# Optimization experiments

Hardware: AMD Instinct MI355X
Metric: run time of the kernel (lower is better)

## Reference

```python
import jax, jax.numpy as jnp
import numpy as np

N, F_IN, H, C = 100000, 256, 128, 64
E, EP = 1600000, 500000


def setup_inputs() -> dict:
    key = jax.random.key(0)
    ks = jax.random.split(key, 8)
    x = jax.random.normal(ks[0], (N, F_IN), jnp.float32)
    masked_nodes = jax.random.randint(ks[1], (1000,), 0, N)
    pos_edge_index = jax.random.randint(ks[2], (2, EP), 0, N)
    neg_edge_index = jax.random.randint(ks[3], (2, EP), 0, N)
    edge_index = jax.random.randint(ks[4], (2, E), 0, N)
    W1 = jax.random.normal(ks[5], (F_IN, H), jnp.float32) / np.sqrt(F_IN).astype(np.float32)
    b1 = jnp.zeros((H,), jnp.float32)
    W2 = jax.random.normal(ks[6], (H, C), jnp.float32) / np.sqrt(H).astype(np.float32)
    b2 = jnp.zeros((C,), jnp.float32)
    return dict(x=x, masked_nodes=masked_nodes, pos_edge_index=pos_edge_index,
                neg_edge_index=neg_edge_index, edge_index=edge_index,
                W1=W1, b1=b1, W2=W2, b2=b2)


def gcn_conv(x, W, b, src, dst, n):
    # PyG GCNConv: h = x @ W; symmetric norm with self-loops; aggregate; + bias
    h = x @ W  # [N, out]
    deg = jax.ops.segment_sum(jnp.ones(src.shape[0], h.dtype), dst, num_segments=n) + 1.0
    dis = jax.lax.rsqrt(deg)  # D^{-1/2} including self-loop
    msg = h[src] * (dis[src] * dis[dst])[:, None]           # gather + edge-norm
    agg = jax.ops.segment_sum(msg, dst, num_segments=n)      # scatter-add
    agg = agg + h * (dis * dis)[:, None]                      # self-loop term
    return agg + b


def reference(x, masked_nodes, pos_edge_index, neg_edge_index, edge_index, W1, b1, W2, b2):
    n = x.shape[0]
    src, dst = edge_index[0], edge_index[1]
    h = jax.nn.relu(gcn_conv(x, W1, b1, src, dst, n))
    h = gcn_conv(h, W2, b2, src, dst, n)  # [N, C]
    tei = jnp.concatenate([pos_edge_index, neg_edge_index], axis=-1)  # [2, 2*EP]
    x_j = h[tei[0]]  # [2EP, C]
    x_i = h[tei[1]]
    scores = jnp.einsum('ef,ef->e', x_i, x_j)
    return scores, jnp.zeros(tei.shape, jnp.float32)
```

## Files before the change

kernel.cpp:

```cpp
#include <hip/hip_runtime.h>

#define N_NODES 100000
#define F_IN    256
#define H_DIM   128
#define C_DIM   64
#define E_EDGES 1600000
#define EP_EDGES 500000

#define NBUK 391
#define EPB  4096

typedef unsigned short bf16_t;
typedef short  short8  __attribute__((ext_vector_type(8)));
typedef float  float4v __attribute__((ext_vector_type(4)));

__device__ inline bf16_t f2bf(float f) {
    unsigned u = __float_as_uint(f);
    u += 0x7fff + ((u >> 16) & 1);
    return (bf16_t)(u >> 16);
}
__device__ inline float bf2f(bf16_t h) {
    return __uint_as_float(((unsigned)h) << 16);
}
__device__ inline void split8(const float* vv, short* h, short* l) {
#pragma unroll
    for (int j = 0; j < 8; ++j) {
        bf16_t hb = f2bf(vv[j]);
        h[j] = (short)hb;
        l[j] = (short)f2bf(vv[j] - bf2f(hb));
    }
}
__device__ inline float4v mfma16(short8 a, short8 b, float4v c) {
    return __builtin_amdgcn_mfma_f32_16x16x32_bf16(a, b, c, 0, 0, 0);
}

__global__ __launch_bounds__(256) void hist_kernel(const int* __restrict__ dst,
                                                   int* __restrict__ counts) {
    int e = blockIdx.x * 256 + threadIdx.x;
    if (e < E_EDGES) atomicAdd(&counts[dst[e]], 1);
}

__global__ __launch_bounds__(256) void dis_kernel(const int* __restrict__ counts,
                                                  float* __restrict__ dis) {
    int i = blockIdx.x * 256 + threadIdx.x;
    if (i < N_NODES) dis[i] = rsqrtf((float)counts[i] + 1.0f);
}

__global__ __launch_bounds__(256) void scan1_kernel(const int* __restrict__ counts,
                                                    int* __restrict__ row_ptr,
                                                    int* __restrict__ blocksum) {
    __shared__ int sh[256];
    int t = threadIdx.x;
    int i = blockIdx.x * 256 + t;
    int v = (i < N_NODES) ? counts[i] : 0;
    sh[t] = v;
    __syncthreads();
#pragma unroll
    for (int off = 1; off < 256; off <<= 1) {
        int u = (t >= off) ? sh[t - off] : 0;
        __syncthreads();
        sh[t] += u;
        __syncthreads();
    }
    if (i < N_NODES) row_ptr[i + 1] = sh[t];
    if (t == 255) blocksum[blockIdx.x] = sh[255];
}

__global__ __launch_bounds__(512) void scan2_kernel(int* __restrict__ blocksum, int nb) {
    __shared__ int sh[512];
    int t = threadIdx.x;
    sh[t] = (t < nb) ? blocksum[t] : 0;
    __syncthreads();
#pragma unroll
    for (int off = 1; off < 512; off <<= 1) {
        int u = (t >= off) ? sh[t - off] : 0;
        __syncthreads();
        sh[t] += u;
        __syncthreads();
    }
    if (t < nb) blocksum[t] = (t == 0) ? 0 : sh[t - 1];
}

__global__ __launch_bounds__(256) void scan3_kernel(int* __restrict__ row_ptr,
                                                    const int* __restrict__ blocksum) {
    int i = blockIdx.x * 256 + threadIdx.x;
    if (i >= N_NODES) return;
    row_ptr[i + 1] += blocksum[blockIdx.x];
    if (i == 0) row_ptr[0] = 0;
}

__global__ __launch_bounds__(512) void binit_kernel(const int* __restrict__ row_ptr,
                                                    int* __restrict__ bcursor) {
    int b = threadIdx.x;
    if (b < NBUK) bcursor[b] = row_ptr[b << 8];
}

__global__ __launch_bounds__(256) void bucket_scatter_kernel(const int* __restrict__ src,
                                                             const int* __restrict__ dst,
                                                             int* __restrict__ bcursor,
                                                             int2* __restrict__ pairs) {
    __shared__ int hist[NBUK];
    __shared__ int base[NBUK];
    const int t = threadIdx.x;
    for (int b = t; b < NBUK; b += 256) hist[b] = 0;
    __syncthreads();

    const int e0 = blockIdx.x * EPB;
    int s[16], d[16];
#pragma unroll
    for (int i = 0; i < 16; ++i) {
        int e = e0 + i * 256 + t;
        if (e < E_EDGES) {
            s[i] = src[e];
            d[i] = dst[e];
            atomicAdd(&hist[d[i] >> 8], 1);
        } else {
            d[i] = -1;
        }
    }
    __syncthreads();
    for (int b = t; b < NBUK; b += 256) {
        int c = hist[b];
        base[b] = c ? atomicAdd(&bcursor[b], c) : 0;
        hist[b] = 0;
    }
    __syncthreads();
#pragma unroll
    for (int i = 0; i < 16; ++i) {
        if (d[i] >= 0) {
            int b = d[i] >> 8;
            int r = atomicAdd(&hist[b], 1);
            pairs[base[b] + r] = make_int2(s[i], d[i]);
        }
    }
}

__global__ __launch_bounds__(256) void bucket_sort_kernel(const int2* __restrict__ pairs,
                                                          const int* __restrict__ row_ptr,
                                                          int* __restrict__ csr_src) {
    __shared__ int cursor[256];
    const int b = blockIdx.x;
    const int node0 = b << 8;
    const int t = threadIdx.x;
    const int nn = min(256, N_NODES - node0);
    if (t < nn) cursor[t] = row_ptr[node0 + t];
    __syncthreads();
    const int beg = row_ptr[node0];
    const int end = row_ptr[node0 + nn];
    for (int e = beg + t; e < end; e += 256) {
        int2 p = pairs[e];
        int j = atomicAdd(&cursor[p.y - node0], 1);
        csr_src[j] = p.x;
    }
}

__global__ __launch_bounds__(256) void wprep_kernel(const float* __restrict__ W1,
                                                    const float* __restrict__ W2,
                                                    short* __restrict__ w1h,
                                                    short* __restrict__ w1l,
                                                    short* __restrict__ w2h,
                                                    short* __restrict__ w2l) {
    int idx = blockIdx.x * 256 + threadIdx.x;
    if (idx < H_DIM * F_IN) {
        int n = idx >> 8, k = idx & 255;
        float w = W1[k * H_DIM + n];
        bf16_t h = f2bf(w);
        w1h[idx] = (short)h;
        w1l[idx] = (short)f2bf(w - bf2f(h));
    }
    int i2 = idx - H_DIM * F_IN;
    if (i2 >= 0 && i2 < C_DIM * H_DIM) {
        int n = i2 >> 7, k = i2 & 127;
        float w = W2[k * C_DIM + n];
        bf16_t h = f2bf(w);
        w2h[i2] = (short)h;
        w2l[i2] = (short)f2bf(w - bf2f(h));
    }
}

__global__ __launch_bounds__(256) void gemm1_mfma(const float* __restrict__ X,
                                                  const short* __restrict__ Wth,
                                                  const short* __restrict__ Wtl,
                                                  bf16_t* __restrict__ T,
                                                  int nrows) {
    __shared__ short Ah[128 * 48], Al[128 * 48];
    __shared__ short Bh[128 * 48], Bl[128 * 48];
    const int t = threadIdx.x;
    const int row0 = blockIdx.x * 128;
    const int w = t >> 6;
    const int lane = t & 63;
    const int m = lane & 15;
    const int q = lane >> 4;
    const int koff = q * 8;

    float4v acc[2][8];
#pragma unroll
    for (int i = 0; i < 2; ++i)
#pragma unroll
        for (int j = 0; j < 8; ++j) acc[i][j] = {0.f, 0.f, 0.f, 0.f};

    for (int ks = 0; ks < 8; ++ks) {
        const int k0 = ks * 32;
#pragma unroll
        for (int i = 0; i < 2; ++i) {
            int c = t + i * 256;
            int r = c >> 2, kc = c & 3;
            int row = row0 + r;
            float vv[8] = {0.f, 0.f, 0.f, 0.f, 0.f, 0.f, 0.f, 0.f};
            if (row < nrows) {
                float4 v0 = *(const float4*)&X[(long long)row * F_IN + k0 + kc * 8];
                float4 v1 = *(const float4*)&X[(long long)row * F_IN + k0 + kc * 8 + 4];
                vv[0] = v0.x; vv[1] = v0.y; vv[2] = v0.z; vv[3] = v0.w;
                vv[4] = v1.x; vv[5] = v1.y; vv[6] = v1.z; vv[7] = v1.w;
            }
            short h[8], l[8];
            split8(vv, h, l);
            *(short8*)&Ah[r * 48 + kc * 8] = *(short8*)h;
            *(short8*)&Al[r * 48 + kc * 8] = *(short8*)l;
        }
#pragma unroll
        for (int i = 0; i < 2; ++i) {
            int c = t + i * 256;
            int n = c >> 2, kc = c & 3;
            *(short8*)&Bh[n * 48 + kc * 8] = *(const short8*)&Wth[n * F_IN + k0 + kc * 8];
            *(short8*)&Bl[n * 48 + kc * 8] = *(const short8*)&Wtl[n * F_IN + k0 + kc * 8];
        }
        __syncthreads();

        short8 ah0 = *(const short8*)&Ah[(w * 32 + m) * 48 + koff];
        short8 ah1 = *(const short8*)&Ah[(w * 32 + 16 + m) * 48 + koff];
        short8 al0 = *(const short8*)&Al[(w * 32 + m) * 48 + koff];
        short8 al1 = *(const short8*)&Al[(w * 32 + 16 + m) * 48 + koff];
#pragma unroll
        for (int nc = 0; nc < 8; ++nc) {
            short8 bh = *(const short8*)&Bh[(nc * 16 + m) * 48 + koff];
            short8 bl = *(const short8*)&Bl[(nc * 16 + m) * 48 + koff];
            acc[0][nc] = mfma16(ah0, bh, acc[0][nc]);
            acc[0][nc] = mfma16(al0, bh, acc[0][nc]);
            acc[0][nc] = mfma16(ah0, bl, acc[0][nc]);
            acc[1][nc] = mfma16(ah1, bh, acc[1][nc]);
            acc[1][nc] = mfma16(al1, bh, acc[1][nc]);
            acc[1][nc] = mfma16(ah1, bl, acc[1][nc]);
        }
        __syncthreads();
    }
#pragma unroll
    for (int mt = 0; mt < 2; ++mt)
#pragma unroll
        for (int nc = 0; nc < 8; ++nc)
#pragma unroll
            for (int reg = 0; reg < 4; ++reg) {
                int grow = row0 + w * 32 + mt * 16 + q * 4 + reg;
                int gcol = nc * 16 + m;
                if (grow < nrows)
                    T[(long long)grow * H_DIM + gcol] = f2bf(acc[mt][nc][reg]);
            }
}

__global__ __launch_bounds__(256) void gemm2_mfma(const float* __restrict__ A,
                                                  const float* __restrict__ b1,
                                                  const short* __restrict__ Wth,
                                                  const short* __restrict__ Wtl,
                                                  bf16_t* __restrict__ T,
                                                  int nrows) {
    __shared__ short Ah[128 * 48], Al[128 * 48];
    __shared__ short Bh[64 * 48], Bl[64 * 48];
    const int t = threadIdx.x;
    const int row0 = blockIdx.x * 128;
    const int w = t >> 6;
    const int lane = t & 63;
    const int m = lane & 15;
    const int q = lane >> 4;
    const int koff = q * 8;

    float4v acc[2][4];
#pragma unroll
    for (int i = 0; i < 2; ++i)
#pragma unroll
        for (int j = 0; j < 4; ++j) acc[i][j] = {0.f, 0.f, 0.f, 0.f};

    for (int ks = 0; ks < 4; ++ks) {
        const int k0 = ks * 32;
#pragma unroll
        for (int i = 0; i < 2; ++i) {
            int c = t + i * 256;
            int r = c >> 2, kc = c & 3;
            int row = row0 + r;
            float vv[8] = {0.f, 0.f, 0.f, 0.f, 0.f, 0.f, 0.f, 0.f};
            if (row < nrows) {
                float4 v0 = *(const float4*)&A[(long long)row * H_DIM + k0 + kc * 8];
                float4 v1 = *(const float4*)&A[(long long)row * H_DIM + k0 + kc * 8 + 4];
                float4 b0 = *(const float4*)&b1[k0 + kc * 8];
                float4 b1v = *(const float4*)&b1[k0 + kc * 8 + 4];
                vv[0] = fmaxf(v0.x + b0.x, 0.f);  vv[1] = fmaxf(v0.y + b0.y, 0.f);
                vv[2] = fmaxf(v0.z + b0.z, 0.f);  vv[3] = fmaxf(v0.w + b0.w, 0.f);
                vv[4] = fmaxf(v1.x + b1v.x, 0.f); vv[5] = fmaxf(v1.y + b1v.y, 0.f);
                vv[6] = fmaxf(v1.z + b1v.z, 0.f); vv[7] = fmaxf(v1.w + b1v.w, 0.f);
            }
            short h[8], l[8];
            split8(vv, h, l);
            *(short8*)&Ah[r * 48 + kc * 8] = *(short8*)h;
            *(short8*)&Al[r * 48 + kc * 8] = *(short8*)l;
        }
        {
            int n = t >> 2, kc = t & 3;
            *(short8*)&Bh[n * 48 + kc * 8] = *(const short8*)&Wth[n * H_DIM + k0 + kc * 8];
            *(short8*)&Bl[n * 48 + kc * 8] = *(const short8*)&Wtl[n * H_DIM + k0 + kc * 8];
        }
        __syncthreads();

        short8 ah0 = *(const short8*)&Ah[(w * 32 + m) * 48 + koff];
        short8 ah1 = *(const short8*)&Ah[(w * 32 + 16 + m) * 48 + koff];
        short8 al0 = *(const short8*)&Al[(w * 32 + m) * 48 + koff];
        short8 al1 = *(const short8*)&Al[(w * 32 + 16 + m) * 48 + koff];
#pragma unroll
        for (int nc = 0; nc < 4; ++nc) {
            short8 bh = *(const short8*)&Bh[(nc * 16 + m) * 48 + koff];
            short8 bl = *(const short8*)&Bl[(nc * 16 + m) * 48 + koff];
            acc[0][nc] = mfma16(ah0, bh, acc[0][nc]);
            acc[0][nc] = mfma16(al0, bh, acc[0][nc]);
            acc[0][nc] = mfma16(ah0, bl, acc[0][nc]);
            acc[1][nc] = mfma16(ah1, bh, acc[1][nc]);
            acc[1][nc] = mfma16(al1, bh, acc[1][nc]);
            acc[1][nc] = mfma16(ah1, bl, acc[1][nc]);
        }
        __syncthreads();
    }
#pragma unroll
    for (int mt = 0; mt < 2; ++mt)
#pragma unroll
        for (int nc = 0; nc < 4; ++nc)
#pragma unroll
            for (int reg = 0; reg < 4; ++reg) {
                int grow = row0 + w * 32 + mt * 16 + q * 4 + reg;
                int gcol = nc * 16 + m;
                if (grow < nrows)
                    T[(long long)grow * C_DIM + gcol] = f2bf(acc[mt][nc][reg]);
            }
}

__device__ inline void fma8_bf16(float* acc, uint4 u, float c) {
#pragma unroll
    for (int p = 0; p < 4; ++p) {
        unsigned w = (&u.x)[p];
        float lo = __uint_as_float(w << 16);
        float hi = __uint_as_float(w & 0xffff0000u);
        acc[2 * p]     = fmaf(lo, c, acc[2 * p]);
        acc[2 * p + 1] = fmaf(hi, c, acc[2 * p + 1]);
    }
}

template <int CS, bool HAS_BIAS>
__global__ __launch_bounds__(256) void agg_kernel(const bf16_t* __restrict__ t,
                                                  const float* __restrict__ dis,
                                                  const int* __restrict__ row_ptr,
                                                  const int* __restrict__ csr_src,
                                                  const float* __restrict__ bias,
                                                  float* __restrict__ agg) {
    unsigned idx = blockIdx.x * 256u + threadIdx.x;
    if (idx >= (unsigned)(N_NODES << CS)) return;
    int node = idx >> CS;
    int q = idx & ((1 << CS) - 1);
    const uint4* tv = (const uint4*)t;
    float dd = dis[node];
    int beg = row_ptr[node], end = row_ptr[node + 1];

    float acc[8];
#pragma unroll
    for (int p = 0; p < 8; ++p) acc[p] = 0.0f;
    fma8_bf16(acc, tv[idx], dd * dd);

    int j = beg;
    for (; j + 3 < end; j += 4) {
        int s0 = csr_src[j + 0], s1 = csr_src[j + 1];
        int s2 = csr_src[j + 2], s3 = csr_src[j + 3];
        float c0 = dis[s0] * dd, c1 = dis[s1] * dd;
        float c2 = dis[s2] * dd, c3 = dis[s3] * dd;
        uint4 u0 = tv[((unsigned)s0 << CS) + q];
        uint4 u1 = tv[((unsigned)s1 << CS) + q];
        uint4 u2 = tv[((unsigned)s2 << CS) + q];
        uint4 u3 = tv[((unsigned)s3 << CS) + q];
        fma8_bf16(acc, u0, c0);
        fma8_bf16(acc, u1, c1);
        fma8_bf16(acc, u2, c2);
        fma8_bf16(acc, u3, c3);
    }
    for (; j < end; ++j) {
        int s = csr_src[j];
        float c = dis[s] * dd;
        fma8_bf16(acc, tv[((unsigned)s << CS) + q], c);
    }

    if (HAS_BIAS) {
        float4 bv0 = ((const float4*)bias)[q * 2];
        float4 bv1 = ((const float4*)bias)[q * 2 + 1];
        acc[0] += bv0.x; acc[1] += bv0.y; acc[2] += bv0.z; acc[3] += bv0.w;
        acc[4] += bv1.x; acc[5] += bv1.y; acc[6] += bv1.z; acc[7] += bv1.w;
    }
    float4 o0 = make_float4(acc[0], acc[1], acc[2], acc[3]);
    float4 o1 = make_float4(acc[4], acc[5], acc[6], acc[7]);
    ((float4*)agg)[idx * 2]     = o0;
    ((float4*)agg)[idx * 2 + 1] = o1;
}

__global__ __launch_bounds__(256) void score_kernel(const float* __restrict__ h2,
                                                    const int* __restrict__ pos,
                                                    const int* __restrict__ neg,
                                                    float* __restrict__ out) {
    int tid = blockIdx.x * 256 + threadIdx.x;
    int e = tid >> 4;
    int q = tid & 15;
    if (e >= 2 * EP_EDGES) return;
    int i, j;
    if (e < EP_EDGES) {
        j = pos[e];
        i = pos[EP_EDGES + e];
    } else {
        j = neg[e - EP_EDGES];
        i = neg[e];
    }
    float4 a = ((const float4*)h2)[i * (C_DIM / 4) + q];
    float4 b = ((const float4*)h2)[j * (C_DIM / 4) + q];
    float v = a.x * b.x + a.y * b.y + a.z * b.z + a.w * b.w;
    v += __shfl_down(v, 8, 16);
    v += __shfl_down(v, 4, 16);
    v += __shfl_down(v, 2, 16);
    v += __shfl_down(v, 1, 16);
    if (q == 0) out[e] = v;
}

extern "C" void kernel_launch(void* const* d_in, const int* in_sizes, int n_in,
                              void* d_out, int out_size, void* d_ws, size_t ws_size,
                              hipStream_t stream) {
    const float* x  = (const float*)d_in[0];
    const int* pos  = (const int*)d_in[2];
    const int* neg  = (const int*)d_in[3];
    const int* ei   = (const int*)d_in[4];
    const float* W1 = (const float*)d_in[5];
    const float* b1 = (const float*)d_in[6];
    const float* W2 = (const float*)d_in[7];
    const float* b2 = (const float*)d_in[8];
    float* out = (float*)d_out;

    char* ws = (char*)d_ws;
    float*  dis     = (float*) (ws + 0);
    int*    row_ptr = (int*)   (ws + 400000);
    int*    bcursor = (int*)   (ws + 800128);
    int*    csr_src = (int*)   (ws + 801792);
    int2*   pairs   = (int2*)  (ws + 7201792);
    bf16_t* t       = (bf16_t*)(ws + 20001792);
    float*  agg     = (float*) (ws + 45601792);
    short*  w1th    = (short*) (ws + 96801792);
    short*  w1tl    = (short*) (ws + 96867328);
    short*  w2th    = (short*) (ws + 96932864);
    short*  w2tl    = (short*) (ws + 96949248);
    int* counts   = (int*)agg;
    int* blocksum = (int*)agg + 131072;

    const int* esrc = ei;
    const int* edst = ei + E_EDGES;
    const int NB = (N_NODES + 255) / 256;

    hipMemsetAsync(counts, 0, N_NODES * sizeof(int), stream);
    hist_kernel<<<E_EDGES / 256, 256, 0, stream>>>(edst, counts);
    dis_kernel<<<NB, 256, 0, stream>>>(counts, dis);
    scan1_kernel<<<NB, 256, 0, stream>>>(counts, row_ptr, blocksum);
    scan2_kernel<<<1, 512, 0, stream>>>(blocksum, NB);
    scan3_kernel<<<NB, 256, 0, stream>>>(row_ptr, blocksum);
    binit_kernel<<<1, 512, 0, stream>>>(row_ptr, bcursor);
    bucket_scatter_kernel<<<(E_EDGES + EPB - 1) / EPB, 256, 0, stream>>>(
        esrc, edst, bcursor, pairs);
    bucket_sort_kernel<<<NBUK, 256, 0, stream>>>(pairs, row_ptr, csr_src);
    wprep_kernel<<<(H_DIM * F_IN + C_DIM * H_DIM + 255) / 256, 256, 0, stream>>>(
        W1, W2, w1th, w1tl, w2th, w2tl);

    gemm1_mfma<<<(N_NODES + 127) / 128, 256, 0, stream>>>(x, w1th, w1tl, t, N_NODES);
    agg_kernel<4, false><<<(N_NODES * 16 + 255) / 256, 256, 0, stream>>>(
        t, dis, row_ptr, csr_src, nullptr, agg);

    gemm2_mfma<<<(N_NODES + 127) / 128, 256, 0, stream>>>(agg, b1, w2th, w2tl, t, N_NODES);
    agg_kernel<3, true><<<(N_NODES * 8 + 255) / 256, 256, 0, stream>>>(
        t, dis, row_ptr, csr_src, b2, agg);

    score_kernel<<<(2 * EP_EDGES * 16) / 256, 256, 0, stream>>>(agg, pos, neg, out);

    hipMemsetAsync(out + 2 * EP_EDGES, 0, (size_t)4 * EP_EDGES * sizeof(float), stream);
}
```

Measured before the change: 491.1 us.

## Build CSR via bucket-level histogram and per-bucket local counting and scan

The CSR build no longer uses a global per-node atomic histogram followed by a three-kernel scan. It now computes a bucket-level histogram with shared-memory atomics, scans the 391 bucket sizes in one block, and has the bucket sort kernel count per-node degrees locally, scan them, and write row_ptr and dis itself. This removes several launches and the contended global atomics on counts. Separately, the LDS row stride in both GEMM kernels drops from 48 to 40 shorts, changing the shared-memory footprint and bank mapping.

```diff
diff --git a/kernel.cpp b/kernel.cpp
--- a/kernel.cpp
+++ b/kernel.cpp
@@ -34,42 +34,29 @@
     return __builtin_amdgcn_mfma_f32_16x16x32_bf16(a, b, c, 0, 0, 0);
 }
 
-__global__ __launch_bounds__(256) void hist_kernel(const int* __restrict__ dst,
-                                                   int* __restrict__ counts) {
-    int e = blockIdx.x * 256 + threadIdx.x;
-    if (e < E_EDGES) atomicAdd(&counts[dst[e]], 1);
-}
-
-__global__ __launch_bounds__(256) void dis_kernel(const int* __restrict__ counts,
-                                                  float* __restrict__ dis) {
-    int i = blockIdx.x * 256 + threadIdx.x;
-    if (i < N_NODES) dis[i] = rsqrtf((float)counts[i] + 1.0f);
-}
-
-__global__ __launch_bounds__(256) void scan1_kernel(const int* __restrict__ counts,
-                                                    int* __restrict__ row_ptr,
-                                                    int* __restrict__ blocksum) {
-    __shared__ int sh[256];
-    int t = threadIdx.x;
-    int i = blockIdx.x * 256 + t;
-    int v = (i < N_NODES) ? counts[i] : 0;
-    sh[t] = v;
-    __syncthreads();
-#pragma unroll
-    for (int off = 1; off < 256; off <<= 1) {
-        int u = (t >= off) ? sh[t - off] : 0;
-        __syncthreads();
-        sh[t] += u;
-        __syncthreads();
-    }
-    if (i < N_NODES) row_ptr[i + 1] = sh[t];
-    if (t == 255) blocksum[blockIdx.x] = sh[255];
-}
-
-__global__ __launch_bounds__(512) void scan2_kernel(int* __restrict__ blocksum, int nb) {
+__global__ __launch_bounds__(256) void bhist_kernel(const int* __restrict__ dst,
+                                                    int* __restrict__ bsize) {
+    __shared__ int hist[NBUK];
+    const int t = threadIdx.x;
+    for (int b = t; b < NBUK; b += 256) hist[b] = 0;
+    __syncthreads();
+    const int e0 = blockIdx.x * EPB;
+#pragma unroll
+    for (int i = 0; i < 16; ++i) {
+        int e = e0 + i * 256 + t;
+        if (e < E_EDGES) atomicAdd(&hist[dst[e] >> 8], 1);
+    }
+    __syncthreads();
+    for (int b = t; b < NBUK; b += 256)
+        if (hist[b]) atomicAdd(&bsize[b], hist[b]);
+}
+
+__global__ __launch_bounds__(512) void bscan_kernel(const int* __restrict__ bsize,
+                                                    int* __restrict__ bbase,
+                                                    int* __restrict__ bcursor) {
     __shared__ int sh[512];
     int t = threadIdx.x;
-    sh[t] = (t < nb) ? blocksum[t] : 0;
+    sh[t] = (t < NBUK) ? bsize[t] : 0;
     __syncthreads();
 #pragma unroll
     for (int off = 1; off < 512; off <<= 1) {
@@ -78,21 +65,12 @@
         sh[t] += u;
         __syncthreads();
     }
-    if (t < nb) blocksum[t] = (t == 0) ? 0 : sh[t - 1];
-}
-
-__global__ __launch_bounds__(256) void scan3_kernel(int* __restrict__ row_ptr,
-                                                    const int* __restrict__ blocksum) {
-    int i = blockIdx.x * 256 + threadIdx.x;
-    if (i >= N_NODES) return;
-    row_ptr[i + 1] += blocksum[blockIdx.x];
-    if (i == 0) row_ptr[0] = 0;
-}
-
-__global__ __launch_bounds__(512) void binit_kernel(const int* __restrict__ row_ptr,
-                                                    int* __restrict__ bcursor) {
-    int b = threadIdx.x;
-    if (b < NBUK) bcursor[b] = row_ptr[b << 8];
+    if (t < NBUK) {
+        int ex = (t == 0) ? 0 : sh[t - 1];
+        bbase[t] = ex;
+        bcursor[t] = ex;
+    }
+    if (t == 0) bbase[NBUK] = E_EDGES;
 }
 
 __global__ __launch_bounds__(256) void bucket_scatter_kernel(const int* __restrict__ src,
@@ -136,20 +114,42 @@
 }
 
 __global__ __launch_bounds__(256) void bucket_sort_kernel(const int2* __restrict__ pairs,
-                                                          const int* __restrict__ row_ptr,
+                                                          const int* __restrict__ bbase,
+                                                          int* __restrict__ row_ptr,
+                                                          float* __restrict__ dis,
                                                           int* __restrict__ csr_src) {
-    __shared__ int cursor[256];
+    __shared__ int cnt[256];
+    __shared__ int sh[256];
+    __shared__ int cur[256];
     const int b = blockIdx.x;
     const int node0 = b << 8;
     const int t = threadIdx.x;
     const int nn = min(256, N_NODES - node0);
-    if (t < nn) cursor[t] = row_ptr[node0 + t];
-    __syncthreads();
-    const int beg = row_ptr[node0];
-    const int end = row_ptr[node0 + nn];
+    const int beg = bbase[b], end = bbase[b + 1];
+    cnt[t] = 0;
+    __syncthreads();
+    for (int e = beg + t; e < end; e += 256)
+        atomicAdd(&cnt[pairs[e].y - node0], 1);
+    __syncthreads();
+    int c = cnt[t];
+    if (t < nn) dis[node0 + t] = rsqrtf((float)c + 1.0f);
+    sh[t] = c;
+    __syncthreads();
+#pragma unroll
+    for (int off = 1; off < 256; off <<= 1) {
+        int u = (t >= off) ? sh[t - off] : 0;
+        __syncthreads();
+        sh[t] += u;
+        __syncthreads();
+    }
+    int start = beg + sh[t] - c;
+    if (t < nn) row_ptr[node0 + t] = start;
+    cur[t] = start;
+    if (b == NBUK - 1 && t == 0) row_ptr[N_NODES] = E_EDGES;
+    __syncthreads();
     for (int e = beg + t; e < end; e += 256) {
         int2 p = pairs[e];
-        int j = atomicAdd(&cursor[p.y - node0], 1);
+        int j = atomicAdd(&cur[p.y - node0], 1);
         csr_src[j] = p.x;
     }
 }
@@ -178,13 +178,14 @@
     }
 }
 
+#define LSTR 40
 __global__ __launch_bounds__(256) void gemm1_mfma(const float* __restrict__ X,
                                                   const short* __restrict__ Wth,
                                                   const short* __restrict__ Wtl,
                                                   bf16_t* __restrict__ T,
                                                   int nrows) {
-    __shared__ short Ah[128 * 48], Al[128 * 48];
-    __shared__ short Bh[128 * 48], Bl[128 * 48];
+    __shared__ short Ah[128 * LSTR], Al[128 * LSTR];
+    __shared__ short Bh[128 * LSTR], Bl[128 * LSTR];
     const int t = threadIdx.x;
     const int row0 = blockIdx.x * 128;
     const int w = t >> 6;
@@ -215,26 +216,26 @@
             }
             short h[8], l[8];
             split8(vv, h, l);
-            *(short8*)&Ah[r * 48 + kc * 8] = *(short8*)h;
-            *(short8*)&Al[r * 48 + kc * 8] = *(short8*)l;
+            *(short8*)&Ah[r * LSTR + kc * 8] = *(short8*)h;
+            *(short8*)&Al[r * LSTR + kc * 8] = *(short8*)l;
         }
 #pragma unroll
         for (int i = 0; i < 2; ++i) {
             int c = t + i * 256;
             int n = c >> 2, kc = c & 3;
-            *(short8*)&Bh[n * 48 + kc * 8] = *(const short8*)&Wth[n * F_IN + k0 + kc * 8];
-            *(short8*)&Bl[n * 48 + kc * 8] = *(const short8*)&Wtl[n * F_IN + k0 + kc * 8];
-        }
-        __syncthreads();
-
-        short8 ah0 = *(const short8*)&Ah[(w * 32 + m) * 48 + koff];
-        short8 ah1 = *(const short8*)&Ah[(w * 32 + 16 + m) * 48 + koff];
-        short8 al0 = *(const short8*)&Al[(w * 32 + m) * 48 + koff];
-        short8 al1 = *(const short8*)&Al[(w * 32 + 16 + m) * 48 + koff];
+            *(short8*)&Bh[n * LSTR + kc * 8] = *(const short8*)&Wth[n * F_IN + k0 + kc * 8];
+            *(short8*)&Bl[n * LSTR + kc * 8] = *(const short8*)&Wtl[n * F_IN + k0 + kc * 8];
+        }
+        __syncthreads();
+
+        short8 ah0 = *(const short8*)&Ah[(w * 32 + m) * LSTR + koff];
+        short8 ah1 = *(const short8*)&Ah[(w * 32 + 16 + m) * LSTR + koff];
+        short8 al0 = *(const short8*)&Al[(w * 32 + m) * LSTR + koff];
+        short8 al1 = *(const short8*)&Al[(w * 32 + 16 + m) * LSTR + koff];
 #pragma unroll
         for (int nc = 0; nc < 8; ++nc) {
-            short8 bh = *(const short8*)&Bh[(nc * 16 + m) * 48 + koff];
-            short8 bl = *(const short8*)&Bl[(nc * 16 + m) * 48 + koff];
+            short8 bh = *(const short8*)&Bh[(nc * 16 + m) * LSTR + koff];
+            short8 bl = *(const short8*)&Bl[(nc * 16 + m) * LSTR + koff];
             acc[0][nc] = mfma16(ah0, bh, acc[0][nc]);
             acc[0][nc] = mfma16(al0, bh, acc[0][nc]);
             acc[0][nc] = mfma16(ah0, bl, acc[0][nc]);
@@ -263,8 +264,8 @@
                                                   const short* __restrict__ Wtl,
                                                   bf16_t* __restrict__ T,
                                                   int nrows) {
-    __shared__ short Ah[128 * 48], Al[128 * 48];
-    __shared__ short Bh[64 * 48], Bl[64 * 48];
+    __shared__ short Ah[128 * LSTR], Al[128 * LSTR];
+    __shared__ short Bh[64 * LSTR], Bl[64 * LSTR];
     const int t = threadIdx.x;
     const int row0 = blockIdx.x * 128;
     const int w = t >> 6;
@@ -299,24 +300,24 @@
             }
             short h[8], l[8];
             split8(vv, h, l);
-            *(short8*)&Ah[r * 48 + kc * 8] = *(short8*)h;
-            *(short8*)&Al[r * 48 + kc * 8] = *(short8*)l;
+            *(short8*)&Ah[r * LSTR + kc * 8] = *(short8*)h;
+            *(short8*)&Al[r * LSTR + kc * 8] = *(short8*)l;
         }
         {
             int n = t >> 2, kc = t & 3;
-            *(short8*)&Bh[n * 48 + kc * 8] = *(const short8*)&Wth[n * H_DIM + k0 + kc * 8];
-            *(short8*)&Bl[n * 48 + kc * 8] = *(const short8*)&Wtl[n * H_DIM + k0 + kc * 8];
-        }
-        __syncthreads();
-
-        short8 ah0 = *(const short8*)&Ah[(w * 32 + m) * 48 + koff];
-        short8 ah1 = *(const short8*)&Ah[(w * 32 + 16 + m) * 48 + koff];
-        short8 al0 = *(const short8*)&Al[(w * 32 + m) * 48 + koff];
-        short8 al1 = *(const short8*)&Al[(w * 32 + 16 + m) * 48 + koff];
+            *(short8*)&Bh[n * LSTR + kc * 8] = *(const short8*)&Wth[n * H_DIM + k0 + kc * 8];
+            *(short8*)&Bl[n * LSTR + kc * 8] = *(const short8*)&Wtl[n * H_DIM + k0 + kc * 8];
+        }
+        __syncthreads();
+
+        short8 ah0 = *(const short8*)&Ah[(w * 32 + m) * LSTR + koff];
+        short8 ah1 = *(const short8*)&Ah[(w * 32 + 16 + m) * LSTR + koff];
+        short8 al0 = *(const short8*)&Al[(w * 32 + m) * LSTR + koff];
+        short8 al1 = *(const short8*)&Al[(w * 32 + 16 + m) * LSTR + koff];
 #pragma unroll
         for (int nc = 0; nc < 4; ++nc) {
-            short8 bh = *(const short8*)&Bh[(nc * 16 + m) * 48 + koff];
-            short8 bl = *(const short8*)&Bl[(nc * 16 + m) * 48 + koff];
+            short8 bh = *(const short8*)&Bh[(nc * 16 + m) * LSTR + koff];
+            short8 bl = *(const short8*)&Bl[(nc * 16 + m) * LSTR + koff];
             acc[0][nc] = mfma16(ah0, bh, acc[0][nc]);
             acc[0][nc] = mfma16(al0, bh, acc[0][nc]);
             acc[0][nc] = mfma16(ah0, bl, acc[0][nc]);
@@ -445,32 +446,27 @@
     char* ws = (char*)d_ws;
     float*  dis     = (float*) (ws + 0);
     int*    row_ptr = (int*)   (ws + 400000);
-    int*    bcursor = (int*)   (ws + 800128);
-    int*    csr_src = (int*)   (ws + 801792);
-    int2*   pairs   = (int2*)  (ws + 7201792);
-    bf16_t* t       = (bf16_t*)(ws + 20001792);
-    float*  agg     = (float*) (ws + 45601792);
-    short*  w1th    = (short*) (ws + 96801792);
-    short*  w1tl    = (short*) (ws + 96867328);
-    short*  w2th    = (short*) (ws + 96932864);
-    short*  w2tl    = (short*) (ws + 96949248);
-    int* counts   = (int*)agg;
-    int* blocksum = (int*)agg + 131072;
+    int*    bsize   = (int*)   (ws + 800128);
+    int*    bbase   = (int*)   (ws + 801792);
+    int*    bcursor = (int*)   (ws + 803456);
+    int*    csr_src = (int*)   (ws + 805120);
+    int2*   pairs   = (int2*)  (ws + 7205120);
+    bf16_t* t       = (bf16_t*)(ws + 20005120);
+    float*  agg     = (float*) (ws + 45605120);
+    short*  w1th    = (short*) (ws + 96805120);
+    short*  w1tl    = (short*) (ws + 96870656);
+    short*  w2th    = (short*) (ws + 96936192);
+    short*  w2tl    = (short*) (ws + 96952576);
 
     const int* esrc = ei;
     const int* edst = ei + E_EDGES;
-    const int NB = (N_NODES + 255) / 256;
-
-    hipMemsetAsync(counts, 0, N_NODES * sizeof(int), stream);
-    hist_kernel<<<E_EDGES / 256, 256, 0, stream>>>(edst, counts);
-    dis_kernel<<<NB, 256, 0, stream>>>(counts, dis);
-    scan1_kernel<<<NB, 256, 0, stream>>>(counts, row_ptr, blocksum);
-    scan2_kernel<<<1, 512, 0, stream>>>(blocksum, NB);
-    scan3_kernel<<<NB, 256, 0, stream>>>(row_ptr, blocksum);
-    binit_kernel<<<1, 512, 0, stream>>>(row_ptr, bcursor);
+
+    hipMemsetAsync(bsize, 0, NBUK * sizeof(int), stream);
+    bhist_kernel<<<(E_EDGES + EPB - 1) / EPB, 256, 0, stream>>>(edst, bsize);
+    bscan_kernel<<<1, 512, 0, stream>>>(bsize, bbase, bcursor);
     bucket_scatter_kernel<<<(E_EDGES + EPB - 1) / EPB, 256, 0, stream>>>(
         esrc, edst, bcursor, pairs);
-    bucket_sort_kernel<<<NBUK, 256, 0, stream>>>(pairs, row_ptr, csr_src);
+    bucket_sort_kernel<<<NBUK, 256, 0, stream>>>(pairs, bbase, row_ptr, dis, csr_src);
     wprep_kernel<<<(H_DIM * F_IN + C_DIM * H_DIM + 255) / 256, 256, 0, stream>>>(
         W1, W2, w1th, w1tl, w2th, w2tl);
 
```

Result: faster. 438.8 us (-10.7%).
